# Kernel tuning notes

Hardware: AMD Instinct MI355X
Metric: run time of the kernel (lower is better)

Reference implementation:

```python
import jax, jax.numpy as jnp
import numpy as np

T, A, H = 1024, 64, 2048

def setup_inputs() -> dict:
    key = jax.random.key(0)
    ks = jax.random.split(key, 12)
    s = 0.02
    return {
        "actions": jax.random.normal(ks[0], (T, A), jnp.float32),
        "state": jnp.zeros((1, H), jnp.float32),
        "W_ih": jax.random.normal(ks[1], (3 * H, A), jnp.float32) * s,
        "W_hh": jax.random.normal(ks[2], (3 * H, H), jnp.float32) * s,
        "b_ih": jax.random.normal(ks[3], (3 * H,), jnp.float32) * s,
        "b_hh": jax.random.normal(ks[4], (3 * H,), jnp.float32) * s,
        "fc1_w": jax.random.normal(ks[5], (H, H), jnp.float32) * s,
        "fc1_b": jax.random.normal(ks[6], (H,), jnp.float32) * s,
        "fc2_w": jax.random.normal(ks[7], (H, H), jnp.float32) * s,
        "fc2_b": jax.random.normal(ks[8], (H,), jnp.float32) * s,
        "mean_w": jax.random.normal(ks[9], (H, H), jnp.float32) * s,
        "mean_b": jnp.zeros((H,), jnp.float32),
        "std_w": jax.random.normal(ks[10], (H, H), jnp.float32) * s,
        "std_b": jnp.zeros((H,), jnp.float32),
    }

def reference(actions, state, W_ih, W_hh, b_ih, b_hh, fc1_w, fc1_b, fc2_w, fc2_b, mean_w, mean_b, std_w, std_b):
    def step(h, x):
        # torch GRUCell gate order: r, z, n
        gi = x[None] @ W_ih.T + b_ih          # [1, 3H]
        gh = h @ W_hh.T + b_hh                # [1, 3H]
        i_r, i_z, i_n = jnp.split(gi, 3, axis=-1)
        h_r, h_z, h_n = jnp.split(gh, 3, axis=-1)
        r = jax.nn.sigmoid(i_r + h_r)
        z = jax.nn.sigmoid(i_z + h_z)
        n = jnp.tanh(i_n + r * h_n)
        h_new = (1.0 - z) * n + z * h         # [1, H]
        s = jax.nn.elu(h_new)
        s = jax.nn.elu(s @ fc1_w.T + fc1_b)
        s = jax.nn.elu(s @ fc2_w.T + fc2_b)   # carried state for next step
        m = (s @ mean_w.T + mean_b)[0]        # [H]
        sd = jax.nn.softplus(s @ std_w.T + std_b)[0]
        return s, (m, sd)

    _, (means, stds) = jax.lax.scan(step, state, actions)
    return means, stds  # Normal(means, stds) parameters, each [T, H]
```

## Files before the change

### kernel.cpp

```cpp
#include <hip/hip_runtime.h>
#include <hip/hip_bf16.h>
#include <math.h>

#define T_STEPS 1024
#define HDIM    2048
#define ADIM    64
#define NBLK    256
#define NTHR    512
#define WPB     (NTHR / 64)

__device__ __forceinline__ float elu_f(float x)      { return x > 0.f ? x : expm1f(x); }
__device__ __forceinline__ float sigmoid_f(float x)  { return 1.f / (1.f + expf(-x)); }
__device__ __forceinline__ float softplus_f(float x) { return x > 0.f ? x + log1pf(expf(-x)) : log1pf(expf(x)); }

__device__ __forceinline__ float cloadf(const float* p) {
    return __hip_atomic_load(p, __ATOMIC_RELAXED, __HIP_MEMORY_SCOPE_AGENT);
}
__device__ __forceinline__ void cstoref(float* p, float v) {
    __hip_atomic_store(p, v, __ATOMIC_RELAXED, __HIP_MEMORY_SCOPE_AGENT);
}
__device__ __forceinline__ unsigned cloadu(const unsigned* p) {
    return __hip_atomic_load(p, __ATOMIC_RELAXED, __HIP_MEMORY_SCOPE_AGENT);
}
__device__ __forceinline__ void cstoreu(unsigned* p, unsigned v) {
    __hip_atomic_store(p, v, __ATOMIC_RELAXED, __HIP_MEMORY_SCOPE_AGENT);
}

__device__ __forceinline__ void grid_barrier(unsigned* flags, unsigned* gen, unsigned ticket) {
    asm volatile("s_waitcnt vmcnt(0)" ::: "memory");
    __syncthreads();
    if (threadIdx.x == 0) cstoreu(&flags[blockIdx.x], ticket);
    if (blockIdx.x == 0 && threadIdx.x < 64) {
        const int l = threadIdx.x;
        for (;;) {
            unsigned f0 = cloadu(&flags[l]);
            unsigned f1 = cloadu(&flags[l + 64]);
            unsigned f2 = cloadu(&flags[l + 128]);
            unsigned f3 = cloadu(&flags[l + 192]);
            bool ok = (f0 >= ticket) && (f1 >= ticket) && (f2 >= ticket) && (f3 >= ticket);
            if (__all(ok)) break;
        }
        if (l == 0) cstoreu(gen, ticket);
    }
    if (threadIdx.x == 0) {
        while (cloadu(gen) < ticket) {  }
    }
    __syncthreads();
}

__global__ void __launch_bounds__(NTHR, 2) gru_seq_kernel(
    const float* __restrict__ actions, const float* __restrict__ state,
    const float* __restrict__ W_ih, const float* __restrict__ W_hh,
    const float* __restrict__ b_ih, const float* __restrict__ b_hh,
    const float* __restrict__ fc1_w, const float* __restrict__ fc1_b,
    const float* __restrict__ fc2_w, const float* __restrict__ fc2_b,
    float* __restrict__ s_all, float* __restrict__ s0buf, float* __restrict__ s1buf,
    unsigned* flags, unsigned* gen)
{
    __shared__ float lsv[HDIM];
    const int lane = threadIdx.x & 63;
    const int wave = threadIdx.x >> 6;
    const int j    = blockIdx.x * WPB + wave;

    float4 wr[8], wz[8], wn[8], f1[8], f2[8];
    {
        const float4* p0 = (const float4*)(W_hh + (size_t)j * HDIM);
        const float4* p1 = (const float4*)(W_hh + (size_t)(HDIM + j) * HDIM);
        const float4* p2 = (const float4*)(W_hh + (size_t)(2 * HDIM + j) * HDIM);
        const float4* p3 = (const float4*)(fc1_w + (size_t)j * HDIM);
        const float4* p4 = (const float4*)(fc2_w + (size_t)j * HDIM);
        #pragma unroll
        for (int i = 0; i < 8; ++i) {
            wr[i] = p0[i * 64 + lane];
            wz[i] = p1[i * 64 + lane];
            wn[i] = p2[i * 64 + lane];
            f1[i] = p3[i * 64 + lane];
            f2[i] = p4[i * 64 + lane];
        }
    }
    const float wih_r = W_ih[(size_t)j * ADIM + lane];
    const float wih_z = W_ih[(size_t)(HDIM + j) * ADIM + lane];
    const float wih_n = W_ih[(size_t)(2 * HDIM + j) * ADIM + lane];
    const float bias_r = b_ih[j] + b_hh[j];
    const float bias_z = b_ih[HDIM + j] + b_hh[HDIM + j];
    const float bihn   = b_ih[2 * HDIM + j];
    const float bhhn   = b_hh[2 * HDIM + j];
    const float fb1    = fc1_b[j];
    const float fb2    = fc2_b[j];

    const float4* ls4 = (const float4*)lsv;
    unsigned ticket = 0;

    for (int t = 0; t < T_STEPS; ++t) {
        {
            const float* sp = (t == 0) ? state : (s_all + (size_t)(t - 1) * HDIM);
            #pragma unroll
            for (int q = 0; q < 4; ++q)
                lsv[threadIdx.x + q * NTHR] = cloadf(sp + threadIdx.x + q * NTHR);
            __syncthreads();

            float dr = 0.f, dz = 0.f, dnH = 0.f;
            #pragma unroll
            for (int i = 0; i < 8; ++i) {
                const float4 s4 = ls4[i * 64 + lane];
                dr  += s4.x * wr[i].x + s4.y * wr[i].y + s4.z * wr[i].z + s4.w * wr[i].w;
                dz  += s4.x * wz[i].x + s4.y * wz[i].y + s4.z * wz[i].z + s4.w * wz[i].w;
                dnH += s4.x * wn[i].x + s4.y * wn[i].y + s4.z * wn[i].z + s4.w * wn[i].w;
            }
            const float av = actions[t * ADIM + lane];
            dr += av * wih_r;
            dz += av * wih_z;
            float dnA = av * wih_n;
            #pragma unroll
            for (int m = 32; m > 0; m >>= 1) {
                dr  += __shfl_xor(dr, m, 64);
                dz  += __shfl_xor(dz, m, 64);
                dnH += __shfl_xor(dnH, m, 64);
                dnA += __shfl_xor(dnA, m, 64);
            }
            if (lane == 0) {
                const float r  = sigmoid_f(dr + bias_r);
                const float z  = sigmoid_f(dz + bias_z);
                const float n  = tanhf(dnA + bihn + r * (dnH + bhhn));
                const float hp = lsv[j];
                const float hn = (1.f - z) * n + z * hp;
                cstoref(&s0buf[j], elu_f(hn));
            }
        }
        grid_barrier(flags, gen, ++ticket);

        {
            #pragma unroll
            for (int q = 0; q < 4; ++q)
                lsv[threadIdx.x + q * NTHR] = cloadf(s0buf + threadIdx.x + q * NTHR);
            __syncthreads();
            float d1 = 0.f;
            #pragma unroll
            for (int i = 0; i < 8; ++i) {
                const float4 s4 = ls4[i * 64 + lane];
                d1 += s4.x * f1[i].x + s4.y * f1[i].y + s4.z * f1[i].z + s4.w * f1[i].w;
            }
            #pragma unroll
            for (int m = 32; m > 0; m >>= 1) d1 += __shfl_xor(d1, m, 64);
            if (lane == 0) cstoref(&s1buf[j], elu_f(d1 + fb1));
        }
        grid_barrier(flags, gen, ++ticket);

        {
            #pragma unroll
            for (int q = 0; q < 4; ++q)
                lsv[threadIdx.x + q * NTHR] = cloadf(s1buf + threadIdx.x + q * NTHR);
            __syncthreads();
            float d2 = 0.f;
            #pragma unroll
            for (int i = 0; i < 8; ++i) {
                const float4 s4 = ls4[i * 64 + lane];
                d2 += s4.x * f2[i].x + s4.y * f2[i].y + s4.z * f2[i].z + s4.w * f2[i].w;
            }
            #pragma unroll
            for (int m = 32; m > 0; m >>= 1) d2 += __shfl_xor(d2, m, 64);
            if (lane == 0) cstoref(&s_all[(size_t)t * HDIM + j], elu_f(d2 + fb2));
        }
        grid_barrier(flags, gen, ++ticket);
    }
}

__global__ void __launch_bounds__(256) head_gemm_kernel(
    const float* __restrict__ s_all,
    const float* __restrict__ mean_w, const float* __restrict__ mean_b,
    const float* __restrict__ std_w,  const float* __restrict__ std_b,
    float* __restrict__ out)
{
    __shared__ float As[32 * 64];
    __shared__ float Bs[32 * 64];

    const int n0 = blockIdx.x * 64;
    const int t0 = blockIdx.y * 64;
    const bool is_std = (n0 >= HDIM);
    const float* W    = is_std ? std_w : mean_w;
    const float* bias = is_std ? std_b : mean_b;
    const int j0 = is_std ? (n0 - HDIM) : n0;

    const int tid = threadIdx.x;
    const int tx = tid & 15;
    const int ty = tid >> 4;

    float acc[4][4] = {};

    for (int k0 = 0; k0 < HDIM; k0 += 32) {
        __syncthreads();
        #pragma unroll
        for (int p = 0; p < 2; ++p) {
            const int id = tid + p * 256;
            const int m  = id >> 3;
            const int kk = id & 7;
            const float4 a = *(const float4*)&s_all[(size_t)(t0 + m) * HDIM + k0 + kk * 4];
            As[(kk * 4 + 0) * 64 + m] = a.x;
            As[(kk * 4 + 1) * 64 + m] = a.y;
            As[(kk * 4 + 2) * 64 + m] = a.z;
            As[(kk * 4 + 3) * 64 + m] = a.w;
            const float4 b = *(const float4*)&W[(size_t)(j0 + m) * HDIM + k0 + kk * 4];
            Bs[(kk * 4 + 0) * 64 + m] = b.x;
            Bs[(kk * 4 + 1) * 64 + m] = b.y;
            Bs[(kk * 4 + 2) * 64 + m] = b.z;
            Bs[(kk * 4 + 3) * 64 + m] = b.w;
        }
        __syncthreads();

        #pragma unroll
        for (int k = 0; k < 32; ++k) {
            const float4 a = *(const float4*)&As[k * 64 + ty * 4];
            const float4 b = *(const float4*)&Bs[k * 64 + tx * 4];
            const float am[4] = {a.x, a.y, a.z, a.w};
            const float bn[4] = {b.x, b.y, b.z, b.w};
            #pragma unroll
            for (int i = 0; i < 4; ++i)
                #pragma unroll
                for (int jj = 0; jj < 4; ++jj)
                    acc[i][jj] += am[i] * bn[jj];
        }
    }

    const size_t off = is_std ? (size_t)T_STEPS * HDIM : 0;
    #pragma unroll
    for (int i = 0; i < 4; ++i) {
        const int tt = t0 + ty * 4 + i;
        const int jc = j0 + tx * 4;
        float4 v;
        float* vp = (float*)&v;
        #pragma unroll
        for (int jj = 0; jj < 4; ++jj) {
            float val = acc[i][jj] + bias[jc + jj];
            if (is_std) val = softplus_f(val);
            vp[jj] = val;
        }
        *(float4*)&out[off + (size_t)tt * HDIM + jc] = v;
    }
}

extern "C" void kernel_launch(void* const* d_in, const int* in_sizes, int n_in,
                              void* d_out, int out_size, void* d_ws, size_t ws_size,
                              hipStream_t stream) {
    (void)in_sizes; (void)n_in; (void)out_size; (void)ws_size;
    const float* actions = (const float*)d_in[0];
    const float* state   = (const float*)d_in[1];
    const float* W_ih    = (const float*)d_in[2];
    const float* W_hh    = (const float*)d_in[3];
    const float* b_ih    = (const float*)d_in[4];
    const float* b_hh    = (const float*)d_in[5];
    const float* fc1_w   = (const float*)d_in[6];
    const float* fc1_b   = (const float*)d_in[7];
    const float* fc2_w   = (const float*)d_in[8];
    const float* fc2_b   = (const float*)d_in[9];
    const float* mean_w  = (const float*)d_in[10];
    const float* mean_b  = (const float*)d_in[11];
    const float* std_w   = (const float*)d_in[12];
    const float* std_b   = (const float*)d_in[13];
    float* out = (float*)d_out;

    float* s_all = (float*)d_ws;
    float* s0    = s_all + (size_t)T_STEPS * HDIM;
    float* s1    = s0 + HDIM;
    unsigned* flags = (unsigned*)(s1 + HDIM);
    unsigned* gen   = flags + 256 + 32;

    hipMemsetAsync(flags, 0, (256 + 64) * sizeof(unsigned), stream);

    void* args[] = { &actions, &state, &W_ih, &W_hh, &b_ih, &b_hh,
                     &fc1_w, &fc1_b, &fc2_w, &fc2_b,
                     &s_all, &s0, &s1, &flags, &gen };
    hipLaunchCooperativeKernel((const void*)gru_seq_kernel,
                               dim3(NBLK), dim3(NTHR), args, 0, stream);

    dim3 grid(4096 / 64, T_STEPS / 64);
    head_gemm_kernel<<<grid, 256, 0, stream>>>(s_all, mean_w, mean_b, std_w, std_b, out);
}
```

Baseline: 12.38 ms.

## Replace grid barriers with tag-packed dataflow polling on per-element values

```diff
diff --git a/kernel.cpp b/kernel.cpp
--- a/kernel.cpp
+++ b/kernel.cpp
@@ -13,40 +13,36 @@
 __device__ __forceinline__ float sigmoid_f(float x)  { return 1.f / (1.f + expf(-x)); }
 __device__ __forceinline__ float softplus_f(float x) { return x > 0.f ? x + log1pf(expf(-x)) : log1pf(expf(x)); }
 
-__device__ __forceinline__ float cloadf(const float* p) {
+__device__ __forceinline__ unsigned long long cload64(const unsigned long long* p) {
     return __hip_atomic_load(p, __ATOMIC_RELAXED, __HIP_MEMORY_SCOPE_AGENT);
 }
-__device__ __forceinline__ void cstoref(float* p, float v) {
+__device__ __forceinline__ void cstore64(unsigned long long* p, unsigned long long v) {
     __hip_atomic_store(p, v, __ATOMIC_RELAXED, __HIP_MEMORY_SCOPE_AGENT);
 }
-__device__ __forceinline__ unsigned cloadu(const unsigned* p) {
-    return __hip_atomic_load(p, __ATOMIC_RELAXED, __HIP_MEMORY_SCOPE_AGENT);
-}
-__device__ __forceinline__ void cstoreu(unsigned* p, unsigned v) {
-    __hip_atomic_store(p, v, __ATOMIC_RELAXED, __HIP_MEMORY_SCOPE_AGENT);
-}
-
-__device__ __forceinline__ void grid_barrier(unsigned* flags, unsigned* gen, unsigned ticket) {
-    asm volatile("s_waitcnt vmcnt(0)" ::: "memory");
+__device__ __forceinline__ unsigned long long pack_tag(unsigned tag, float v) {
+    return ((unsigned long long)tag << 32) | (unsigned long long)__float_as_uint(v);
+}
+
+__device__ __forceinline__ void consume_vec(const unsigned long long* __restrict__ tg,
+                                            unsigned tag, float* __restrict__ lsv) {
+    const int i = threadIdx.x;
+    unsigned pend = 0xFu;
+    while (pend) {
+        #pragma unroll
+        for (int q = 0; q < 4; ++q) {
+            if (pend & (1u << q)) {
+                const unsigned long long x = cload64(tg + i + q * NTHR);
+                if ((unsigned)(x >> 32) == tag) {
+                    lsv[i + q * NTHR] = __uint_as_float((unsigned)x);
+                    pend &= ~(1u << q);
+                }
+            }
+        }
+    }
     __syncthreads();
-    if (threadIdx.x == 0) cstoreu(&flags[blockIdx.x], ticket);
-    if (blockIdx.x == 0 && threadIdx.x < 64) {
-        const int l = threadIdx.x;
-        for (;;) {
-            unsigned f0 = cloadu(&flags[l]);
-            unsigned f1 = cloadu(&flags[l + 64]);
-            unsigned f2 = cloadu(&flags[l + 128]);
-            unsigned f3 = cloadu(&flags[l + 192]);
-            bool ok = (f0 >= ticket) && (f1 >= ticket) && (f2 >= ticket) && (f3 >= ticket);
-            if (__all(ok)) break;
-        }
-        if (l == 0) cstoreu(gen, ticket);
-    }
-    if (threadIdx.x == 0) {
-        while (cloadu(gen) < ticket) {  }
-    }
-    __syncthreads();
-}
+}
+
+#define KEEP4(v) asm volatile("" : "+v"(v.x), "+v"(v.y), "+v"(v.z), "+v"(v.w))
 
 __global__ void __launch_bounds__(NTHR, 2) gru_seq_kernel(
     const float* __restrict__ actions, const float* __restrict__ state,
@@ -54,8 +50,10 @@
     const float* __restrict__ b_ih, const float* __restrict__ b_hh,
     const float* __restrict__ fc1_w, const float* __restrict__ fc1_b,
     const float* __restrict__ fc2_w, const float* __restrict__ fc2_b,
-    float* __restrict__ s_all, float* __restrict__ s0buf, float* __restrict__ s1buf,
-    unsigned* flags, unsigned* gen)
+    float* __restrict__ s_all,
+    unsigned long long* __restrict__ tg0,
+    unsigned long long* __restrict__ tg1,
+    unsigned long long* __restrict__ tg2)
 {
     __shared__ float lsv[HDIM];
     const int lane = threadIdx.x & 63;
@@ -71,11 +69,11 @@
         const float4* p4 = (const float4*)(fc2_w + (size_t)j * HDIM);
         #pragma unroll
         for (int i = 0; i < 8; ++i) {
-            wr[i] = p0[i * 64 + lane];
-            wz[i] = p1[i * 64 + lane];
-            wn[i] = p2[i * 64 + lane];
-            f1[i] = p3[i * 64 + lane];
-            f2[i] = p4[i * 64 + lane];
+            wr[i] = p0[i * 64 + lane]; KEEP4(wr[i]);
+            wz[i] = p1[i * 64 + lane]; KEEP4(wz[i]);
+            wn[i] = p2[i * 64 + lane]; KEEP4(wn[i]);
+            f1[i] = p3[i * 64 + lane]; KEEP4(f1[i]);
+            f2[i] = p4[i * 64 + lane]; KEEP4(f2[i]);
         }
     }
     const float wih_r = W_ih[(size_t)j * ADIM + lane];
@@ -89,16 +87,20 @@
     const float fb2    = fc2_b[j];
 
     const float4* ls4 = (const float4*)lsv;
-    unsigned ticket = 0;
 
     for (int t = 0; t < T_STEPS; ++t) {
+        const unsigned base = 3u * (unsigned)t;
+
+        const float av = actions[t * ADIM + lane];
+        if (t == 0) {
+            #pragma unroll
+            for (int q = 0; q < 4; ++q)
+                lsv[threadIdx.x + q * NTHR] = state[threadIdx.x + q * NTHR];
+            __syncthreads();
+        } else {
+            consume_vec(tg2, base, lsv);
+        }
         {
-            const float* sp = (t == 0) ? state : (s_all + (size_t)(t - 1) * HDIM);
-            #pragma unroll
-            for (int q = 0; q < 4; ++q)
-                lsv[threadIdx.x + q * NTHR] = cloadf(sp + threadIdx.x + q * NTHR);
-            __syncthreads();
-
             float dr = 0.f, dz = 0.f, dnH = 0.f;
             #pragma unroll
             for (int i = 0; i < 8; ++i) {
@@ -107,10 +109,9 @@
                 dz  += s4.x * wz[i].x + s4.y * wz[i].y + s4.z * wz[i].z + s4.w * wz[i].w;
                 dnH += s4.x * wn[i].x + s4.y * wn[i].y + s4.z * wn[i].z + s4.w * wn[i].w;
             }
-            const float av = actions[t * ADIM + lane];
+            float dnA = av * wih_n;
             dr += av * wih_r;
             dz += av * wih_z;
-            float dnA = av * wih_n;
             #pragma unroll
             for (int m = 32; m > 0; m >>= 1) {
                 dr  += __shfl_xor(dr, m, 64);
@@ -124,16 +125,13 @@
                 const float n  = tanhf(dnA + bihn + r * (dnH + bhhn));
                 const float hp = lsv[j];
                 const float hn = (1.f - z) * n + z * hp;
-                cstoref(&s0buf[j], elu_f(hn));
-            }
-        }
-        grid_barrier(flags, gen, ++ticket);
-
+                cstore64(&tg0[j], pack_tag(base + 1u, elu_f(hn)));
+            }
+        }
+        __syncthreads();
+
+        consume_vec(tg0, base + 1u, lsv);
         {
-            #pragma unroll
-            for (int q = 0; q < 4; ++q)
-                lsv[threadIdx.x + q * NTHR] = cloadf(s0buf + threadIdx.x + q * NTHR);
-            __syncthreads();
             float d1 = 0.f;
             #pragma unroll
             for (int i = 0; i < 8; ++i) {
@@ -142,15 +140,12 @@
             }
             #pragma unroll
             for (int m = 32; m > 0; m >>= 1) d1 += __shfl_xor(d1, m, 64);
-            if (lane == 0) cstoref(&s1buf[j], elu_f(d1 + fb1));
-        }
-        grid_barrier(flags, gen, ++ticket);
-
+            if (lane == 0) cstore64(&tg1[j], pack_tag(base + 2u, elu_f(d1 + fb1)));
+        }
+        __syncthreads();
+
+        consume_vec(tg1, base + 2u, lsv);
         {
-            #pragma unroll
-            for (int q = 0; q < 4; ++q)
-                lsv[threadIdx.x + q * NTHR] = cloadf(s1buf + threadIdx.x + q * NTHR);
-            __syncthreads();
             float d2 = 0.f;
             #pragma unroll
             for (int i = 0; i < 8; ++i) {
@@ -159,9 +154,13 @@
             }
             #pragma unroll
             for (int m = 32; m > 0; m >>= 1) d2 += __shfl_xor(d2, m, 64);
-            if (lane == 0) cstoref(&s_all[(size_t)t * HDIM + j], elu_f(d2 + fb2));
-        }
-        grid_barrier(flags, gen, ++ticket);
+            if (lane == 0) {
+                const float v = elu_f(d2 + fb2);
+                cstore64(&tg2[j], pack_tag(base + 3u, v));
+                s_all[(size_t)t * HDIM + j] = v;
+            }
+        }
+        __syncthreads();
     }
 }
 
@@ -259,16 +258,13 @@
     float* out = (float*)d_out;
 
     float* s_all = (float*)d_ws;
-    float* s0    = s_all + (size_t)T_STEPS * HDIM;
-    float* s1    = s0 + HDIM;
-    unsigned* flags = (unsigned*)(s1 + HDIM);
-    unsigned* gen   = flags + 256 + 32;
-
-    hipMemsetAsync(flags, 0, (256 + 64) * sizeof(unsigned), stream);
+    unsigned long long* tg0 = (unsigned long long*)(s_all + (size_t)T_STEPS * HDIM);
+    unsigned long long* tg1 = tg0 + HDIM;
+    unsigned long long* tg2 = tg1 + HDIM;
 
     void* args[] = { &actions, &state, &W_ih, &W_hh, &b_ih, &b_hh,
                      &fc1_w, &fc1_b, &fc2_w, &fc2_b,
-                     &s_all, &s0, &s1, &flags, &gen };
+                     &s_all, &tg0, &tg1, &tg2 };
     hipLaunchCooperativeKernel((const void*)gru_seq_kernel,
                                dim3(NBLK), dim3(NTHR), args, 0, stream);
 
```

Result: faster. 10.86 ms (-12.3%).
